# Kernel optimization log

Hardware: AMD Instinct MI355X
Metric: run time of the kernel (lower is better)

## Reference

```python
import jax, jax.numpy as jnp
import numpy as np

ITER = 50
SMOOTH = 1e-05


def _max_pool(x, window):
    # x: [B, C, D, H, W]; 'same' max pool with stride 1, -inf padding
    # (matches torch F.max_pool3d semantics with symmetric padding).
    win = (1, 1) + window
    pads = [(0, 0), (0, 0)] + [((w - 1) // 2, (w - 1) // 2) for w in window]
    return jax.lax.reduce_window(x, -jnp.inf, jax.lax.max, win, (1,) * 5, pads)


def soft_erode(img):
    p1 = -_max_pool(-img, (3, 1, 1))
    p2 = -_max_pool(-img, (1, 3, 1))
    p3 = -_max_pool(-img, (1, 1, 3))
    return jnp.minimum(jnp.minimum(p1, p2), p3)


def soft_dilate(img):
    return _max_pool(img, (3, 3, 3))


def soft_open(img):
    return soft_dilate(soft_erode(img))


def soft_skel(img, n_iter):
    skel = jax.nn.relu(img - soft_open(img))

    def body(_, carry):
        img, skel = carry
        img = soft_erode(img)
        delta = jax.nn.relu(img - soft_open(img))
        skel = skel + jax.nn.relu(delta - skel * delta)
        return (img, skel)

    _, skel = jax.lax.fori_loop(0, n_iter, body, (img, skel))
    return skel


def setup_inputs() -> dict:
    key = jax.random.key(0)
    k1, k2 = jax.random.split(key)
    shape = (2, 2, 96, 192, 192)
    pred = jax.random.uniform(k1, shape, dtype=jnp.float32)
    target = jax.random.uniform(k2, shape, dtype=jnp.float32)
    return {"pred": pred, "target": target}


def reference(pred, target):
    pred_fg = pred[:, 1:2, ...]
    target_fg = target[:, 1:2, ...].astype(jnp.float32)
    skel_pred = soft_skel(pred_fg, ITER)
    skel_target = soft_skel(target_fg, ITER)
    tprec = (jnp.sum(skel_pred * target_fg) + SMOOTH) / (jnp.sum(skel_pred) + SMOOTH)
    tsens = (jnp.sum(skel_target * pred_fg) + SMOOTH) / (jnp.sum(skel_target) + SMOOTH)
    cl_dice = 2.0 * (tprec * tsens) / (tprec + tsens + SMOOTH)
    return 1.0 - cl_dice
```

## Files before the change

kernel.cpp:

```cpp
#include <hip/hip_runtime.h>
#include <math.h>

#define NX 192
#define NY 192
#define NZ 96
#define NV 4
#define VOL (NZ * NY * NX)
#define NTOT (NV * VOL)
#define YS NX
#define ZS (NY * NX)

#define TX 48
#define TY2 12
#define ZCH2 16
#define NG 14
#define R2A 18

#define SLOT4(x) (((x) + 100) % 4)
#define SLOT3(x) (((x) + 99) % 3)
#define SLOT2(x) (((x) + 100) % 2)

#define HINF  0x7C00u
#define HNINF 0xFC00u

typedef _Float16 h2v __attribute__((ext_vector_type(2)));

struct __align__(8) H4u { unsigned lo, hi; };

__device__ __forceinline__ h2v h2_of(unsigned u) { return __builtin_bit_cast(h2v, u); }
__device__ __forceinline__ unsigned u_of(h2v h) { return __builtin_bit_cast(unsigned, h); }

__device__ __forceinline__ H4u h4min(H4u a, H4u b) {
    H4u r;
    r.lo = u_of(__builtin_elementwise_min(h2_of(a.lo), h2_of(b.lo)));
    r.hi = u_of(__builtin_elementwise_min(h2_of(a.hi), h2_of(b.hi)));
    return r;
}
__device__ __forceinline__ H4u h4max(H4u a, H4u b) {
    H4u r;
    r.lo = u_of(__builtin_elementwise_max(h2_of(a.lo), h2_of(b.lo)));
    r.hi = u_of(__builtin_elementwise_max(h2_of(a.hi), h2_of(b.hi)));
    return r;
}
__device__ __forceinline__ H4u h4add(H4u a, H4u b) {
    H4u r;
    r.lo = u_of(h2_of(a.lo) + h2_of(b.lo));
    r.hi = u_of(h2_of(a.hi) + h2_of(b.hi));
    return r;
}
__device__ __forceinline__ H4u h4sub(H4u a, H4u b) {
    H4u r;
    r.lo = u_of(h2_of(a.lo) - h2_of(b.lo));
    r.hi = u_of(h2_of(a.hi) - h2_of(b.hi));
    return r;
}
__device__ __forceinline__ H4u h4mul(H4u a, H4u b) {
    H4u r;
    r.lo = u_of(h2_of(a.lo) * h2_of(b.lo));
    r.hi = u_of(h2_of(a.hi) * h2_of(b.hi));
    return r;
}
__device__ __forceinline__ H4u h4skel(H4u s, H4u a, H4u dil) {
    const H4u HZ4 = { 0u, 0u };
    const H4u HONE = { 0x3C003C00u, 0x3C003C00u };
    H4u dd = h4max(h4sub(a, dil), HZ4);
    H4u t = h4mul(dd, h4sub(HONE, s));
    return h4add(s, h4max(t, HZ4));
}
__device__ __forceinline__ H4u shl1(H4u c, unsigned p16) {
    H4u r;
    r.lo = (c.lo << 16) | (p16 & 0xFFFFu);
    r.hi = (c.hi << 16) | (c.lo >> 16);
    return r;
}
__device__ __forceinline__ H4u shr1(H4u c, unsigned n16) {
    H4u r;
    r.lo = (c.lo >> 16) | (c.hi << 16);
    r.hi = (c.hi >> 16) | ((n16 & 0xFFFFu) << 16);
    return r;
}
__device__ __forceinline__ H4u f4_to_h4(float4 f) {
    h2v a, b;
    a[0] = (_Float16)f.x; a[1] = (_Float16)f.y;
    b[0] = (_Float16)f.z; b[1] = (_Float16)f.w;
    H4u r; r.lo = u_of(a); r.hi = u_of(b); return r;
}
__device__ __forceinline__ float4 h4_to_f4(H4u h) {
    h2v a = h2_of(h.lo), b = h2_of(h.hi);
    return make_float4((float)a[0], (float)a[1], (float)b[0], (float)b[1]);
}

template<bool FIRST>
__global__ __launch_bounds__(256, 6) void fused2_kernel(
    const float* __restrict__ pred, const float* __restrict__ target,
    const _Float16* __restrict__ Ain, _Float16* __restrict__ Eout,
    _Float16* __restrict__ skel)
{
    __shared__ H4u As[4][R2A][NG];
    __shared__ H4u E1c[3][16][NG];
    __shared__ H4u ZM1[2][16][NG];
    __shared__ H4u ZM2[2][16][NG];

    const int tid = threadIdx.x;
    const int lr  = tid >> 4;
    const int c   = tid & 15;
    const int cc  = (c < 14) ? c : 13;
    const int sr  = tid / 14;
    const int sg  = tid - sr * 14;

    const int x0 = blockIdx.x * TX;
    const int y0 = blockIdx.y * TY2;
    const int v  = blockIdx.z / 6;
    const int ch = blockIdx.z % 6;
    const int z0 = ch * ZCH2;
    const int z1 = z0 + ZCH2;

    const float* Af = nullptr;
    const _Float16* Ah = nullptr;
    if (FIRST) Af = ((v < 2) ? pred : target) + (size_t)((v & 1) * 2 + 1) * VOL;
    else       Ah = Ain + (size_t)v * VOL;
    _Float16* Ev = Eout + (size_t)v * VOL;
    _Float16* Sv = skel + (size_t)v * VOL;

    const H4u HP4 = { 0x7C007C00u, 0x7C007C00u };
    const H4u HN4 = { 0xFC00FC00u, 0xFC00FC00u };
    const H4u HZ4 = { 0u, 0u };

    const bool xlo = (x0 == 0);
    const bool xhi = (x0 + TX == NX);

    const int  gys  = y0 - 3 + sr;
    const int  gxs  = x0 - 4 + 4 * sg;
    const bool stIn = (sr < R2A) && (gys >= 0) && (gys < NY) &&
                      (gxs >= 0) && (gxs < NX);

    const int  gx   = x0 - 4 + 4 * c;
    const bool gxin = (c < 14) && (gx >= 0) && (gx < NX);
    const int  gyo  = y0 - 2 + lr;
    const bool yIn  = (gyo >= 0) && (gyo < NY);
    const bool uAct = (lr >= 2 && lr <= 13 && c >= 1 && c <= 12);
    const int  rdn  = (lr > 0) ? lr - 1 : 0;
    const int  rup  = (lr < 15) ? lr + 1 : 15;

    auto stageLoad = [&](int za) -> H4u {
        H4u val = HP4;
        if (stIn && za >= 0 && za < NZ) {
            if (FIRST)
                val = f4_to_h4(*(const float4*)(Af + (size_t)za * ZS + gys * YS + gxs));
            else
                val = *(const H4u*)(Ah + (size_t)za * ZS + gys * YS + gxs);
        }
        return val;
    };
    auto stageWrite = [&](int za, H4u val) {
        if (sr < R2A) As[SLOT4(za)][sr][sg] = val;
    };

    auto e1compute = [&](int zp, H4u& cenOut) -> H4u {
        if (zp >= NZ) { cenOut = HP4; return HP4; }
        const int s_c = SLOT4(zp), s_m = SLOT4(zp - 1), s_p = SLOT4(zp + 1);
        const bool hp = (zp + 1 < NZ);
        const int ar = lr + 1;
        H4u cen = As[s_c][ar][cc];
        H4u ylo = As[s_c][ar - 1][cc];
        H4u yhi = As[s_c][ar + 1][cc];
        H4u zlo = As[s_m][ar][cc];
        H4u zhi = hp ? As[s_p][ar][cc] : HP4;
        cenOut = cen;
        unsigned lw = __shfl_up(cen.hi, 1) >> 16;
        unsigned rx = __shfl_down(cen.lo, 1) & 0xFFFFu;
        if (c == 0) lw = HINF;
        H4u m = h4min(cen, shl1(cen, lw));
        m = h4min(m, shr1(cen, rx));
        m = h4min(m, h4min(ylo, yhi));
        m = h4min(m, h4min(zlo, zhi));
        if (zp < 0 || !yIn || !gxin) m = HP4;
        if (c < 14) E1c[SLOT3(zp)][lr][c] = m;
        return m;
    };

    stageWrite(z0 - 3, stageLoad(z0 - 3));
    stageWrite(z0 - 2, stageLoad(z0 - 2));
    stageWrite(z0 - 1, stageLoad(z0 - 1));
    stageWrite(z0,     stageLoad(z0));
    __syncthreads();
    H4u aT, a1, a2 = HP4;
    H4u e1m2 = e1compute(z0 - 2, aT);
    H4u e1m1 = e1compute(z0 - 1, aT);
    __syncthreads();
    stageWrite(z0 + 1, stageLoad(z0 + 1));
    __syncthreads();
    H4u e1c = e1compute(z0, a1);
    stageWrite(z0 + 2, stageLoad(z0 + 2));
    __syncthreads();

    H4u e1m3 = HP4;
    H4u e2c = HN4, e2m1 = HN4;
    H4u zm1_prev = HN4, zm2_prev = HN4;
    H4u skA = HZ4, sq1 = HZ4, sq2 = HZ4;

    for (int z = z0; z <= z1 + 2; ++z) {
        const bool doStage = (z <= z1 - 1);
        H4u stv = doStage ? stageLoad(z + 3) : HP4;
        H4u skN = HZ4;
        if (!FIRST && z < z1 && uAct)
            skN = *(const H4u*)(Sv + (size_t)z * ZS + gyo * YS + gx);

        H4u aC = HP4;
        H4u e1new = (z <= z1) ? e1compute(z + 1, aC) : HP4;

        H4u zm1w;
        {
            H4u t0 = (z >= 1) ? e1m1 : HN4;
            H4u t2 = (z + 1 < NZ) ? e1new : HN4;
            zm1w = h4max(t0, h4max(e1c, t2));
            if (!yIn || !gxin) zm1w = HN4;
            if (c < 14) ZM1[SLOT2(z)][lr][c] = zm1w;
        }

        const int p = z - 1;
        H4u e2new = HN4;
        if (p >= 0 && p <= z1 && p < NZ) {
            H4u cen = e1m1;
            H4u zlo = e1m2;
            H4u zhi = e1c;
            H4u ylo = E1c[SLOT3(p)][rdn][cc];
            H4u yhi = E1c[SLOT3(p)][rup][cc];
            unsigned lwE = __shfl_up(cen.hi, 1) >> 16;
            unsigned rxE = __shfl_down(cen.lo, 1) & 0xFFFFu;
            if (c == 0) lwE = HINF;
            H4u m2 = h4min(cen, shl1(cen, lwE));
            m2 = h4min(m2, shr1(cen, rxE));
            m2 = h4min(m2, h4min(ylo, yhi));
            m2 = h4min(m2, h4min(zlo, zhi));
            if (yIn && gxin) {
                e2new = m2;
                if (p >= z0 && p < z1 && lr >= 2 && lr <= 13 && c >= 1 && c <= 12)
                    *(H4u*)(Ev + (size_t)p * ZS + gyo * YS + gx) = m2;
            }
        }

        H4u zm2w = h4max(e2m1, h4max(e2c, e2new));
        if (c < 14) ZM2[SLOT2(z - 2)][lr][c] = zm2w;

        H4u spnew = HZ4;
        if (p >= z0 && p < z1) {
            H4u vm = h4max(ZM1[SLOT2(p)][rdn][cc],
                     h4max(zm1_prev, ZM1[SLOT2(p)][rup][cc]));
            unsigned lw = __shfl_up(vm.hi, 1) >> 16;
            unsigned rx = __shfl_down(vm.lo, 1) & 0xFFFFu;
            if (xlo && c == 1)  lw = HNINF;
            if (xhi && c == 12) rx = HNINF;
            if (uAct) {
                H4u dilh = h4max(h4max(shl1(vm, lw), vm), shr1(vm, rx));
                spnew = h4skel(skA, a2, dilh);
            }
        }

        const int q = z - 3;
        if (q >= z0 && q < z1) {
            H4u vm2 = h4max(ZM2[SLOT2(q)][rdn][cc],
                      h4max(zm2_prev, ZM2[SLOT2(q)][rup][cc]));
            unsigned lw = __shfl_up(vm2.hi, 1) >> 16;
            unsigned rx = __shfl_down(vm2.lo, 1) & 0xFFFFu;
            if (xlo && c == 1)  lw = HNINF;
            if (xhi && c == 12) rx = HNINF;
            if (uAct) {
                H4u dilh = h4max(h4max(shl1(vm2, lw), vm2), shr1(vm2, rx));
                H4u s = h4skel(sq2, e1m3, dilh);
                *(H4u*)(Sv + (size_t)q * ZS + gyo * YS + gx) = s;
            }
        }

        if (doStage) stageWrite(z + 3, stv);

        __syncthreads();
        e1m3 = e1m2; e1m2 = e1m1; e1m1 = e1c; e1c = e1new;
        e2m1 = e2c; e2c = e2new;
        zm1_prev = zm1w; zm2_prev = zm2w;
        a2 = a1; a1 = aC;
        sq2 = sq1; sq1 = spnew; skA = skN;
    }
}

__global__ __launch_bounds__(256, 6) void last_kernel(
    const _Float16* __restrict__ Ain,
    const float* __restrict__ pred, const float* __restrict__ target,
    const _Float16* __restrict__ skel, double* __restrict__ sums)
{
    __shared__ H4u As[4][R2A][NG];
    __shared__ H4u ZM1[2][16][NG];
    __shared__ double sred[8];

    const int tid = threadIdx.x;
    const int lr  = tid >> 4;
    const int c   = tid & 15;
    const int cc  = (c < 14) ? c : 13;
    const int sr  = tid / 14;
    const int sg  = tid - sr * 14;

    const int x0 = blockIdx.x * TX;
    const int y0 = blockIdx.y * TY2;
    const int v  = blockIdx.z / 6;
    const int ch = blockIdx.z % 6;
    const int z0 = ch * ZCH2;
    const int z1 = z0 + ZCH2;

    const _Float16* Ah = Ain + (size_t)v * VOL;
    const _Float16* Sv = skel + (size_t)v * VOL;
    const float* Ov = ((v < 2) ? target : pred) + (size_t)((v & 1) * 2 + 1) * VOL;

    const H4u HP4 = { 0x7C007C00u, 0x7C007C00u };
    const H4u HN4 = { 0xFC00FC00u, 0xFC00FC00u };
    const H4u HZ4 = { 0u, 0u };
    const float4 ZERO4 = make_float4(0.f, 0.f, 0.f, 0.f);

    const bool xlo = (x0 == 0);
    const bool xhi = (x0 + TX == NX);

    const int  gys  = y0 - 3 + sr;
    const int  gxs  = x0 - 4 + 4 * sg;
    const bool stIn = (sr < R2A) && (gys >= 0) && (gys < NY) &&
                      (gxs >= 0) && (gxs < NX);

    const int  gx   = x0 - 4 + 4 * c;
    const bool gxin = (c < 14) && (gx >= 0) && (gx < NX);
    const int  gyo  = y0 - 2 + lr;
    const bool yIn  = (gyo >= 0) && (gyo < NY);
    const bool uAct = (lr >= 2 && lr <= 13 && c >= 1 && c <= 12);
    const int  rdn  = (lr > 0) ? lr - 1 : 0;
    const int  rup  = (lr < 15) ? lr + 1 : 15;

    auto stageLoad = [&](int za) -> H4u {
        H4u val = HP4;
        if (stIn && za >= 0 && za < NZ)
            val = *(const H4u*)(Ah + (size_t)za * ZS + gys * YS + gxs);
        return val;
    };
    auto stageWrite = [&](int za, H4u val) {
        if (sr < R2A) As[SLOT4(za)][sr][sg] = val;
    };

    auto e1compute = [&](int zp, H4u& cenOut) -> H4u {
        if (zp >= NZ) { cenOut = HP4; return HP4; }
        const int s_c = SLOT4(zp), s_m = SLOT4(zp - 1), s_p = SLOT4(zp + 1);
        const bool hp = (zp + 1 < NZ);
        const int ar = lr + 1;
        H4u cen = As[s_c][ar][cc];
        H4u ylo = As[s_c][ar - 1][cc];
        H4u yhi = As[s_c][ar + 1][cc];
        H4u zlo = As[s_m][ar][cc];
        H4u zhi = hp ? As[s_p][ar][cc] : HP4;
        cenOut = cen;
        unsigned lw = __shfl_up(cen.hi, 1) >> 16;
        unsigned rx = __shfl_down(cen.lo, 1) & 0xFFFFu;
        if (c == 0) lw = HINF;
        H4u m = h4min(cen, shl1(cen, lw));
        m = h4min(m, shr1(cen, rx));
        m = h4min(m, h4min(ylo, yhi));
        m = h4min(m, h4min(zlo, zhi));
        if (zp < 0 || !yIn || !gxin) m = HP4;
        return m;
    };

    stageWrite(z0 - 2, stageLoad(z0 - 2));
    stageWrite(z0 - 1, stageLoad(z0 - 1));
    stageWrite(z0,     stageLoad(z0));
    stageWrite(z0 + 1, stageLoad(z0 + 1));
    __syncthreads();
    H4u aT, a1, a2 = HP4;
    H4u e1m1 = e1compute(z0 - 1, aT);
    H4u e1c  = e1compute(z0, a1);
    __syncthreads();
    stageWrite(z0 + 2, stageLoad(z0 + 2));
    __syncthreads();

    H4u zmP = HN4;
    H4u skA = HZ4;
    float4 oA = ZERO4;
    double afd = 0.0, afs = 0.0;

    for (int z = z0; z <= z1; ++z) {
        const bool doStage = (z <= z1 - 2);
        H4u stv = doStage ? stageLoad(z + 3) : HP4;
        H4u skN = HZ4;
        float4 oN = ZERO4;
        if (z < z1 && uAct) {
            skN = *(const H4u*)(Sv + (size_t)z * ZS + gyo * YS + gx);
            oN  = *(const float4*)(Ov + (size_t)z * ZS + gyo * YS + gx);
        }

        H4u aC = HP4;
        H4u e1new = (z + 1 <= z1) ? e1compute(z + 1, aC) : HP4;

        H4u zm1w = HN4;
        if (z <= z1 - 1) {
            H4u t0 = (z >= 1) ? e1m1 : HN4;
            H4u t2 = (z + 1 < NZ) ? e1new : HN4;
            zm1w = h4max(t0, h4max(e1c, t2));
            if (!yIn || !gxin) zm1w = HN4;
            if (c < 14) ZM1[SLOT2(z)][lr][c] = zm1w;
        }

        const int p = z - 1;
        if (p >= z0 && p < z1) {
            H4u vm = h4max(ZM1[SLOT2(p)][rdn][cc],
                     h4max(zmP, ZM1[SLOT2(p)][rup][cc]));
            unsigned lw = __shfl_up(vm.hi, 1) >> 16;
            unsigned rx = __shfl_down(vm.lo, 1) & 0xFFFFu;
            if (xlo && c == 1)  lw = HNINF;
            if (xhi && c == 12) rx = HNINF;
            if (uAct) {
                H4u dilh = h4max(h4max(shl1(vm, lw), vm), shr1(vm, rx));
                H4u s = h4skel(skA, a2, dilh);
                float4 sf = h4_to_f4(s);
                afd += (double)(sf.x * oA.x + sf.y * oA.y +
                                sf.z * oA.z + sf.w * oA.w);
                afs += (double)(sf.x + sf.y + sf.z + sf.w);
            }
        }

        if (doStage) stageWrite(z + 3, stv);

        __syncthreads();
        e1m1 = e1c; e1c = e1new;
        a2 = a1; a1 = aC;
        zmP = zm1w;
        skA = skN; oA = oN;
    }

#pragma unroll
    for (int off = 32; off > 0; off >>= 1) {
        afd += __shfl_down(afd, off, 64);
        afs += __shfl_down(afs, off, 64);
    }
    int lane = tid & 63, wid = tid >> 6;
    if (lane == 0) { sred[wid * 2] = afd; sred[wid * 2 + 1] = afs; }
    __syncthreads();
    if (tid == 0) {
        double fd = sred[0] + sred[2] + sred[4] + sred[6];
        double fs = sred[1] + sred[3] + sred[5] + sred[7];
        if (v < 2) { atomicAdd(&sums[0], fd); atomicAdd(&sums[1], fs); }
        else       { atomicAdd(&sums[2], fd); atomicAdd(&sums[3], fs); }
    }
}

__global__ void final_kernel(const double* __restrict__ sums,
                             float* __restrict__ out) {
    if (threadIdx.x == 0 && blockIdx.x == 0) {
        const double SM = 1e-5;
        double tprec = (sums[0] + SM) / (sums[1] + SM);
        double tsens = (sums[2] + SM) / (sums[3] + SM);
        double cl = 2.0 * tprec * tsens / (tprec + tsens + SM);
        out[0] = (float)(1.0 - cl);
    }
}

extern "C" void kernel_launch(void* const* d_in, const int* in_sizes, int n_in,
                              void* d_out, int out_size, void* d_ws, size_t ws_size,
                              hipStream_t stream) {
    const float* pred = (const float*)d_in[0];
    const float* target = (const float*)d_in[1];
    float* out = (float*)d_out;

    _Float16* H0 = (_Float16*)d_ws;
    _Float16* H1 = H0 + NTOT;
    _Float16* skel = H1 + NTOT;
    double* sums = (double*)(skel + NTOT);

    hipMemsetAsync(sums, 0, 4 * sizeof(double), stream);

    dim3 dgrid(NX / TX, NY / TY2, NV * 6);

    fused2_kernel<true><<<dgrid, 256, 0, stream>>>(pred, target, H0, H0, skel);
    _Float16* A = H0;
    _Float16* B = H1;
    for (int j = 0; j < 24; ++j) {
        fused2_kernel<false><<<dgrid, 256, 0, stream>>>(pred, target, A, B, skel);
        _Float16* t = A; A = B; B = t;
    }
    last_kernel<<<dgrid, 256, 0, stream>>>(A, pred, target, skel, sums);

    final_kernel<<<1, 64, 0, stream>>>(sums, out);
}
```

Before: 1.444 ms.

## Process two z-slices per loop step with deeper ring buffers and taller chunks

The fused two-erosion kernel now advances two z-planes per iteration, halving the number of block barriers, and uses deeper shared-memory ring buffers (8-slot input staging, 4-slot intermediates) so two planes can be staged at once. Z chunks grow from 16 to 24 planes, which cuts halo recomputation and redundant halo loads, and launch bounds drop to 4 blocks per CU to make room for the larger shared memory and register footprint. The cost is more registers and LDS per block, fewer blocks in the grid (256 instead of 384), and lower occupancy, which may hurt latency hiding.

New measurement: 1.423 ms. No clear change (-1.5%).

```diff
diff --git a/kernel.cpp b/kernel.cpp
--- a/kernel.cpp
+++ b/kernel.cpp
@@ -12,12 +12,14 @@
 
 #define TX 48
 #define TY2 12
-#define ZCH2 16
 #define NG 14
 #define R2A 18
 
+#define ZCHM 24
+#define ZCH2 16
+
+#define SLOT8(x) (((x) + 104) % 8)
 #define SLOT4(x) (((x) + 100) % 4)
-#define SLOT3(x) (((x) + 99) % 3)
 #define SLOT2(x) (((x) + 100) % 2)
 
 #define HINF  0x7C00u
@@ -91,15 +93,15 @@
 }
 
 template<bool FIRST>
-__global__ __launch_bounds__(256, 6) void fused2_kernel(
+__global__ __launch_bounds__(256, 4) void fused2x_kernel(
     const float* __restrict__ pred, const float* __restrict__ target,
     const _Float16* __restrict__ Ain, _Float16* __restrict__ Eout,
     _Float16* __restrict__ skel)
 {
-    __shared__ H4u As[4][R2A][NG];
-    __shared__ H4u E1c[3][16][NG];
-    __shared__ H4u ZM1[2][16][NG];
-    __shared__ H4u ZM2[2][16][NG];
+    __shared__ H4u As[8][R2A][NG];
+    __shared__ H4u E1c[4][16][NG];
+    __shared__ H4u ZM1[4][16][NG];
+    __shared__ H4u ZM2[4][16][NG];
 
     const int tid = threadIdx.x;
     const int lr  = tid >> 4;
@@ -110,10 +112,10 @@
 
     const int x0 = blockIdx.x * TX;
     const int y0 = blockIdx.y * TY2;
-    const int v  = blockIdx.z / 6;
-    const int ch = blockIdx.z % 6;
-    const int z0 = ch * ZCH2;
-    const int z1 = z0 + ZCH2;
+    const int v  = blockIdx.z / 4;
+    const int ch = blockIdx.z % 4;
+    const int z0 = ch * ZCHM;
+    const int z1 = z0 + ZCHM;
 
     const float* Af = nullptr;
     const _Float16* Ah = nullptr;
@@ -153,12 +155,12 @@
         return val;
     };
     auto stageWrite = [&](int za, H4u val) {
-        if (sr < R2A) As[SLOT4(za)][sr][sg] = val;
+        if (sr < R2A) As[SLOT8(za)][sr][sg] = val;
     };
 
     auto e1compute = [&](int zp, H4u& cenOut) -> H4u {
         if (zp >= NZ) { cenOut = HP4; return HP4; }
-        const int s_c = SLOT4(zp), s_m = SLOT4(zp - 1), s_p = SLOT4(zp + 1);
+        const int s_c = SLOT8(zp), s_m = SLOT8(zp - 1), s_p = SLOT8(zp + 1);
         const bool hp = (zp + 1 < NZ);
         const int ar = lr + 1;
         H4u cen = As[s_c][ar][cc];
@@ -175,8 +177,35 @@
         m = h4min(m, h4min(ylo, yhi));
         m = h4min(m, h4min(zlo, zhi));
         if (zp < 0 || !yIn || !gxin) m = HP4;
-        if (c < 14) E1c[SLOT3(zp)][lr][c] = m;
+        if (c < 14) E1c[SLOT4(zp)][lr][c] = m;
         return m;
+    };
+
+    auto e2compute = [&](int p, H4u cen, H4u zlo, H4u zhi) -> H4u {
+        H4u ylo = E1c[SLOT4(p)][rdn][cc];
+        H4u yhi = E1c[SLOT4(p)][rup][cc];
+        unsigned lwE = __shfl_up(cen.hi, 1) >> 16;
+        unsigned rxE = __shfl_down(cen.lo, 1) & 0xFFFFu;
+        if (c == 0) lwE = HINF;
+        H4u m2 = h4min(cen, shl1(cen, lwE));
+        m2 = h4min(m2, shr1(cen, rxE));
+        m2 = h4min(m2, h4min(ylo, yhi));
+        m2 = h4min(m2, h4min(zlo, zhi));
+        H4u res = HN4;
+        if (yIn && gxin) {
+            res = m2;
+            if (p >= z0 && p < z1 && lr >= 2 && lr <= 13 && c >= 1 && c <= 12)
+                *(H4u*)(Ev + (size_t)p * ZS + gyo * YS + gx) = m2;
+        }
+        return res;
+    };
+
+    auto dilateX = [&](H4u vm) -> H4u {
+        unsigned lw = __shfl_up(vm.hi, 1) >> 16;
+        unsigned rx = __shfl_down(vm.lo, 1) & 0xFFFFu;
+        if (xlo && c == 1)  lw = HNINF;
+        if (xhi && c == 12) rx = HNINF;
+        return h4max(h4max(shl1(vm, lw), vm), shr1(vm, rx));
     };
 
     stageWrite(z0 - 3, stageLoad(z0 - 3));
@@ -184,102 +213,117 @@
     stageWrite(z0 - 1, stageLoad(z0 - 1));
     stageWrite(z0,     stageLoad(z0));
     __syncthreads();
-    H4u aT, a1, a2 = HP4;
-    H4u e1m2 = e1compute(z0 - 2, aT);
-    H4u e1m1 = e1compute(z0 - 1, aT);
-    __syncthreads();
+    H4u aDump, aPa, aPb;
+    H4u eP2b = e1compute(z0 - 2, aDump);
+    H4u eP1a = e1compute(z0 - 1, aPa);
     stageWrite(z0 + 1, stageLoad(z0 + 1));
-    __syncthreads();
-    H4u e1c = e1compute(z0, a1);
     stageWrite(z0 + 2, stageLoad(z0 + 2));
-    __syncthreads();
-
-    H4u e1m3 = HP4;
-    H4u e2c = HN4, e2m1 = HN4;
-    H4u zm1_prev = HN4, zm2_prev = HN4;
-    H4u skA = HZ4, sq1 = HZ4, sq2 = HZ4;
-
-    for (int z = z0; z <= z1 + 2; ++z) {
-        const bool doStage = (z <= z1 - 1);
-        H4u stv = doStage ? stageLoad(z + 3) : HP4;
-        H4u skN = HZ4;
-        if (!FIRST && z < z1 && uAct)
-            skN = *(const H4u*)(Sv + (size_t)z * ZS + gyo * YS + gx);
-
-        H4u aC = HP4;
-        H4u e1new = (z <= z1) ? e1compute(z + 1, aC) : HP4;
-
-        H4u zm1w;
+    stageWrite(z0 + 3, stageLoad(z0 + 3));
+    stageWrite(z0 + 4, stageLoad(z0 + 4));
+    __syncthreads();
+    H4u eP1b = e1compute(z0, aPb);
+    __syncthreads();
+
+    H4u e1P3a = HP4, e1P3b = HP4;
+    H4u e1P2a = HP4, e1P2b = eP2b;
+    H4u e1P1a = eP1a, e1P1b = eP1b;
+    H4u aP2a = HP4, aP2b = HP4;
+    H4u aP1a = aPa, aP1b = aPb;
+    H4u e2Pa = HN4, e2Pb = HN4;
+    H4u zm1Pa = HN4, zm1Pb = HN4;
+    H4u zm2Pa = HN4, zm2Pb = HN4;
+    H4u skPa = HZ4, skPb = HZ4;
+    H4u sqPa = HZ4, sqPb = HZ4;
+
+    for (int z = z0; z <= z1 + 2; z += 2) {
+        H4u stv5 = (z + 5 <= z1 + 2) ? stageLoad(z + 5) : HP4;
+        H4u stv6 = (z + 6 <= z1 + 2) ? stageLoad(z + 6) : HP4;
+        H4u skNa = HZ4, skNb = HZ4;
+        if (!FIRST && uAct) {
+            if (z < z1)
+                skNa = *(const H4u*)(Sv + (size_t)z * ZS + gyo * YS + gx);
+            if (z + 1 < z1)
+                skNb = *(const H4u*)(Sv + (size_t)(z + 1) * ZS + gyo * YS + gx);
+        }
+
+        H4u aA = HP4, aB = HP4;
+        H4u e1A = (z + 1 <= z1 + 1) ? e1compute(z + 1, aA) : HP4;
+        H4u e1B = (z + 2 <= z1 + 1) ? e1compute(z + 2, aB) : HP4;
+
+        H4u zm1a, zm1b;
         {
-            H4u t0 = (z >= 1) ? e1m1 : HN4;
-            H4u t2 = (z + 1 < NZ) ? e1new : HN4;
-            zm1w = h4max(t0, h4max(e1c, t2));
-            if (!yIn || !gxin) zm1w = HN4;
-            if (c < 14) ZM1[SLOT2(z)][lr][c] = zm1w;
-        }
-
-        const int p = z - 1;
-        H4u e2new = HN4;
-        if (p >= 0 && p <= z1 && p < NZ) {
-            H4u cen = e1m1;
-            H4u zlo = e1m2;
-            H4u zhi = e1c;
-            H4u ylo = E1c[SLOT3(p)][rdn][cc];
-            H4u yhi = E1c[SLOT3(p)][rup][cc];
-            unsigned lwE = __shfl_up(cen.hi, 1) >> 16;
-            unsigned rxE = __shfl_down(cen.lo, 1) & 0xFFFFu;
-            if (c == 0) lwE = HINF;
-            H4u m2 = h4min(cen, shl1(cen, lwE));
-            m2 = h4min(m2, shr1(cen, rxE));
-            m2 = h4min(m2, h4min(ylo, yhi));
-            m2 = h4min(m2, h4min(zlo, zhi));
-            if (yIn && gxin) {
-                e2new = m2;
-                if (p >= z0 && p < z1 && lr >= 2 && lr <= 13 && c >= 1 && c <= 12)
-                    *(H4u*)(Ev + (size_t)p * ZS + gyo * YS + gx) = m2;
+            H4u t0 = (z >= 1) ? e1P1a : HN4;
+            H4u t2 = (z + 1 < NZ) ? e1A : HN4;
+            zm1a = h4max(t0, h4max(e1P1b, t2));
+            H4u t2b = (z + 2 < NZ) ? e1B : HN4;
+            zm1b = h4max(e1P1b, h4max(e1A, t2b));
+            if (!yIn || !gxin) { zm1a = HN4; zm1b = HN4; }
+            if (c < 14) {
+                ZM1[SLOT4(z)][lr][c] = zm1a;
+                ZM1[SLOT4(z + 1)][lr][c] = zm1b;
             }
         }
 
-        H4u zm2w = h4max(e2m1, h4max(e2c, e2new));
-        if (c < 14) ZM2[SLOT2(z - 2)][lr][c] = zm2w;
-
-        H4u spnew = HZ4;
-        if (p >= z0 && p < z1) {
-            H4u vm = h4max(ZM1[SLOT2(p)][rdn][cc],
-                     h4max(zm1_prev, ZM1[SLOT2(p)][rup][cc]));
-            unsigned lw = __shfl_up(vm.hi, 1) >> 16;
-            unsigned rx = __shfl_down(vm.lo, 1) & 0xFFFFu;
-            if (xlo && c == 1)  lw = HNINF;
-            if (xhi && c == 12) rx = HNINF;
+        H4u e2A = HN4, e2B = HN4;
+        if (z - 1 >= 0 && z - 1 <= z1 && z - 1 < NZ)
+            e2A = e2compute(z - 1, e1P1a, e1P2b, e1P1b);
+        if (z >= 0 && z <= z1 && z < NZ)
+            e2B = e2compute(z, e1P1b, e1P1a, e1A);
+
+        H4u zm2a = h4max(e2Pa, h4max(e2Pb, e2A));
+        H4u zm2b = h4max(e2Pb, h4max(e2A, e2B));
+        if (c < 14) {
+            ZM2[SLOT4(z - 2)][lr][c] = zm2a;
+            ZM2[SLOT4(z - 1)][lr][c] = zm2b;
+        }
+
+        H4u spA = HZ4, spB = HZ4;
+        if (z - 2 >= z0 && z - 2 < z1) {
+            H4u vm = h4max(ZM1[SLOT4(z - 2)][rdn][cc],
+                     h4max(zm1Pa, ZM1[SLOT4(z - 2)][rup][cc]));
+            H4u dil = dilateX(vm);
+            if (uAct) spA = h4skel(skPa, aP2b, dil);
+        }
+        if (z - 1 >= z0 && z - 1 < z1) {
+            H4u vm = h4max(ZM1[SLOT4(z - 1)][rdn][cc],
+                     h4max(zm1Pb, ZM1[SLOT4(z - 1)][rup][cc]));
+            H4u dil = dilateX(vm);
+            if (uAct) spB = h4skel(skPb, aP1a, dil);
+        }
+
+        if (z - 4 >= z0 && z - 4 < z1) {
+            H4u vm2 = h4max(ZM2[SLOT4(z - 4)][rdn][cc],
+                      h4max(zm2Pa, ZM2[SLOT4(z - 4)][rup][cc]));
+            H4u dil = dilateX(vm2);
             if (uAct) {
-                H4u dilh = h4max(h4max(shl1(vm, lw), vm), shr1(vm, rx));
-                spnew = h4skel(skA, a2, dilh);
+                H4u s = h4skel(sqPa, e1P3b, dil);
+                *(H4u*)(Sv + (size_t)(z - 4) * ZS + gyo * YS + gx) = s;
             }
         }
-
-        const int q = z - 3;
-        if (q >= z0 && q < z1) {
-            H4u vm2 = h4max(ZM2[SLOT2(q)][rdn][cc],
-                      h4max(zm2_prev, ZM2[SLOT2(q)][rup][cc]));
-            unsigned lw = __shfl_up(vm2.hi, 1) >> 16;
-            unsigned rx = __shfl_down(vm2.lo, 1) & 0xFFFFu;
-            if (xlo && c == 1)  lw = HNINF;
-            if (xhi && c == 12) rx = HNINF;
+        if (z - 3 >= z0 && z - 3 < z1) {
+            H4u vm2 = h4max(ZM2[SLOT4(z - 3)][rdn][cc],
+                      h4max(zm2Pb, ZM2[SLOT4(z - 3)][rup][cc]));
+            H4u dil = dilateX(vm2);
             if (uAct) {
-                H4u dilh = h4max(h4max(shl1(vm2, lw), vm2), shr1(vm2, rx));
-                H4u s = h4skel(sq2, e1m3, dilh);
-                *(H4u*)(Sv + (size_t)q * ZS + gyo * YS + gx) = s;
+                H4u s = h4skel(sqPb, e1P2a, dil);
+                *(H4u*)(Sv + (size_t)(z - 3) * ZS + gyo * YS + gx) = s;
             }
         }
 
-        if (doStage) stageWrite(z + 3, stv);
+        if (z + 5 <= z1 + 2) stageWrite(z + 5, stv5);
+        if (z + 6 <= z1 + 2) stageWrite(z + 6, stv6);
 
         __syncthreads();
-        e1m3 = e1m2; e1m2 = e1m1; e1m1 = e1c; e1c = e1new;
-        e2m1 = e2c; e2c = e2new;
-        zm1_prev = zm1w; zm2_prev = zm2w;
-        a2 = a1; a1 = aC;
-        sq2 = sq1; sq1 = spnew; skA = skN;
+        e1P3a = e1P2a; e1P3b = e1P2b;
+        e1P2a = e1P1a; e1P2b = e1P1b;
+        e1P1a = e1A;   e1P1b = e1B;
+        aP2a = aP1a; aP2b = aP1b;
+        aP1a = aA;   aP1b = aB;
+        e2Pa = e2A; e2Pb = e2B;
+        zm1Pa = zm1a; zm1Pb = zm1b;
+        zm2Pa = zm2a; zm2Pb = zm2b;
+        skPa = skNa; skPb = skNb;
+        sqPa = spA; sqPb = spB;
     }
 }
 
@@ -470,16 +514,17 @@
 
     hipMemsetAsync(sums, 0, 4 * sizeof(double), stream);
 
-    dim3 dgrid(NX / TX, NY / TY2, NV * 6);
-
-    fused2_kernel<true><<<dgrid, 256, 0, stream>>>(pred, target, H0, H0, skel);
+    dim3 mgrid(NX / TX, NY / TY2, NV * 4);
+    dim3 lgrid(NX / TX, NY / TY2, NV * 6);
+
+    fused2x_kernel<true><<<mgrid, 256, 0, stream>>>(pred, target, H0, H0, skel);
     _Float16* A = H0;
     _Float16* B = H1;
     for (int j = 0; j < 24; ++j) {
-        fused2_kernel<false><<<dgrid, 256, 0, stream>>>(pred, target, A, B, skel);
+        fused2x_kernel<false><<<mgrid, 256, 0, stream>>>(pred, target, A, B, skel);
         _Float16* t = A; A = B; B = t;
     }
-    last_kernel<<<dgrid, 256, 0, stream>>>(A, pred, target, skel, sums);
+    last_kernel<<<lgrid, 256, 0, stream>>>(A, pred, target, skel, sums);
 
     final_kernel<<<1, 64, 0, stream>>>(sums, out);
 }
```
